# Kernel optimization log

Hardware: AMD Instinct MI355X
Metric: run time of the kernel (lower is better)

Reference implementation:

```python
import jax, jax.numpy as jnp
from jax import lax
import numpy as np

B, C, N, MAX_OUT = 8, 16, 2048, 100


def setup_inputs() -> dict:
    key = jax.random.key(0)
    kc, kw, ks = jax.random.split(key, 3)
    # well-formed xyxy boxes: centers in [0,1000), sizes in [1,101)
    ctr = jax.random.uniform(kc, (B, N, 2), jnp.float32) * 1000.0
    wh = jax.random.uniform(kw, (B, N, 2), jnp.float32) * 100.0 + 1.0
    boxes = jnp.concatenate([ctr - wh * 0.5, ctr + wh * 0.5], axis=-1)  # [B,N,4]
    scores = jax.random.uniform(ks, (B, C, N), jnp.float32)  # [B,C,N]
    return {
        "boxes": boxes,
        "scores": scores,
        "max_output_boxes_per_class": MAX_OUT,
        "iou_threshold": jnp.array([0.5], jnp.float32),
        "score_threshold": jnp.array([0.5], jnp.float32),
    }


def _pairwise_iou(bx):
    # bx: [N,4] xyxy -> [N,N] IoU (matches torchvision.ops.box_iou)
    x1, y1, x2, y2 = bx[:, 0], bx[:, 1], bx[:, 2], bx[:, 3]
    area = (x2 - x1) * (y2 - y1)
    iw = jnp.clip(jnp.minimum(x2[:, None], x2[None, :]) - jnp.maximum(x1[:, None], x1[None, :]), 0.0)
    ih = jnp.clip(jnp.minimum(y2[:, None], y2[None, :]) - jnp.maximum(y1[:, None], y1[None, :]), 0.0)
    inter = iw * ih
    return inter / (area[:, None] + area[None, :] - inter)


def _nms_selected(boxes, scores, iou_threshold, score_threshold, max_out):
    # boxes [B,N,4], scores [B,C,N]
    b, c, n = scores.shape
    iou = jax.vmap(_pairwise_iou)(boxes)  # [B,N,N], shared across classes
    iou_t = iou_threshold.reshape(())
    score_t = score_threshold.reshape(())

    def one_class(iou_b, cls_scores):
        order = jnp.argsort(-cls_scores)          # descending score order [N]
        valid = cls_scores[order] > score_t       # strict >, as in the torch code

        def step(suppressed, inp):
            ok, bi = inp
            kept = ok & (~suppressed[bi])
            # greedy suppression: a kept box removes all boxes with IoU > thr
            suppressed = suppressed | (kept & (iou_b[bi] > iou_t))
            return suppressed, kept

        _, keep = lax.scan(step, jnp.zeros((n,), bool), (valid, order))
        rank = jnp.cumsum(keep.astype(jnp.int32)) - 1
        sel = keep & (rank < max_out)
        pos = jnp.where(sel, rank, max_out)  # overflow/non-selected -> dropped slot
        buf = jnp.full((max_out + 1,), -1, jnp.int32).at[pos].set(
            jnp.where(sel, order.astype(jnp.int32), -1))
        return buf[:max_out]  # box indices in score order, -1 padded

    per_bc = jax.vmap(lambda iou_b, sb: jax.vmap(lambda s: one_class(iou_b, s))(sb))(iou, scores)  # [B,C,max_out]
    b_idx = jnp.broadcast_to(jnp.arange(b, dtype=jnp.int32)[:, None, None], per_bc.shape)
    c_idx = jnp.broadcast_to(jnp.arange(c, dtype=jnp.int32)[None, :, None], per_bc.shape)
    rows = jnp.stack([b_idx, c_idx, per_bc], axis=-1).reshape(-1, 3)  # [B*C*max_out, 3]
    # invalid (padded) rows are all -1
    return jnp.where(rows[:, 2:3] >= 0, rows, -1)


def reference(boxes, scores, max_output_boxes_per_class, iou_threshold, score_threshold):
    return _nms_selected(boxes, scores, iou_threshold, score_threshold,
                         int(max_output_boxes_per_class))
```

## Files before the change

kernel.cpp:

```cpp
#include <hip/hip_runtime.h>
#include <stdint.h>


#define NBOX 2048
#define THREADS 1024
#define CHUNK 128
#define MAXKEEP 256

__global__ __launch_bounds__(THREADS) void nms_kernel(
    const float* __restrict__ boxes,
    const float* __restrict__ scores,
    const int* __restrict__ maxOutPtr,
    const float* __restrict__ iouThrPtr,
    const float* __restrict__ scoreThrPtr,
    int* __restrict__ out,
    int B, int C, int slots)
{
  __shared__ unsigned long long skeys[NBOX];
  __shared__ float sx1[NBOX], sy1[NBOX], sx2[NBOX], sy2[NBOX], sar[NBOX];
  __shared__ unsigned colmask[CHUNK][4];
  __shared__ unsigned char suppPre[CHUNK];
  __shared__ int keptPos[MAXKEEP];
  __shared__ int Vsh, cntSh;

  const int tid  = threadIdx.x;
  const int lane = tid & 63;
  const int wave = tid >> 6;
  const int bc = blockIdx.x;
  const int b = bc / C, c = bc % C;
  const float iouT   = iouThrPtr[0];
  const float scoreT = scoreThrPtr[0];
  int mOut = maxOutPtr[0];
  if (mOut > slots) mOut = slots;
  if (mOut > MAXKEEP) mOut = MAXKEEP;
  if (mOut < 0) mOut = 0;

  const float* cls = scores + ((size_t)b * C + c) * NBOX;
  if (tid == 0) { Vsh = 0; cntSh = 0; }
  __syncthreads();

  {
    float s0 = cls[tid], s1 = cls[tid + 1024];
    unsigned u0 = __float_as_uint(s0); u0 = (u0 & 0x80000000u) ? ~u0 : (u0 | 0x80000000u);
    unsigned u1 = __float_as_uint(s1); u1 = (u1 & 0x80000000u) ? ~u1 : (u1 | 0x80000000u);
    skeys[tid]        = ((unsigned long long)u0 << 32) | (0xFFFFFFFFu - (unsigned)tid);
    skeys[tid + 1024] = ((unsigned long long)u1 << 32) | (0xFFFFFFFFu - (unsigned)(tid + 1024));
    unsigned long long m0 = __ballot(s0 > scoreT);
    unsigned long long m1 = __ballot(s1 > scoreT);
    if (lane == 0) atomicAdd(&Vsh, __popcll(m0) + __popcll(m1));
  }

  for (unsigned k = 2; k <= NBOX; k <<= 1) {
    for (unsigned s = k >> 1; s > 0; s >>= 1) {
      __syncthreads();
      unsigned i = ((tid & ~(s - 1)) << 1) | (tid & (s - 1));
      unsigned j = i | s;
      unsigned long long a = skeys[i], bb = skeys[j];
      bool up = ((i & k) == 0);
      bool sw = up ? (a < bb) : (a > bb);
      if (sw) { skeys[i] = bb; skeys[j] = a; }
    }
  }
  __syncthreads();
  const int V = Vsh;

  const float4* bx = (const float4*)boxes + (size_t)b * NBOX;
  for (int p = tid; p < V; p += THREADS) {
    int idx = (int)(0xFFFFFFFFu - (unsigned)skeys[p]);
    float4 f = bx[idx];
    sx1[p] = f.x; sy1[p] = f.y; sx2[p] = f.z; sy2[p] = f.w;
    sar[p] = (f.z - f.x) * (f.w - f.y);
  }
  __syncthreads();

  int cnt = 0;
  for (int s0 = 0; s0 < V && cnt < mOut; s0 += CHUNK) {
    int clen = V - s0; if (clen > CHUNK) clen = CHUNK;

    if (tid < CHUNK * 4) ((unsigned*)colmask)[tid] = 0;
    if (tid < CHUNK) suppPre[tid] = 0;
    __syncthreads();

    {
      int qo = tid & (CHUNK - 1);
      int ko = tid >> 7;
      if (qo < clen) {
        int q = s0 + qo;
        float qx1 = sx1[q], qy1 = sy1[q], qx2 = sx2[q], qy2 = sy2[q], qa = sar[q];
        int hit = 0;
        for (int k = ko; k < cnt; k += 8) {
          int kp = keptPos[k];
          float iw = fminf(sx2[kp], qx2) - fmaxf(sx1[kp], qx1);
          float ih = fminf(sy2[kp], qy2) - fmaxf(sy1[kp], qy1);
          iw = fmaxf(iw, 0.0f); ih = fmaxf(ih, 0.0f);
          float inter = iw * ih;
          float iou = inter / (sar[kp] + qa - inter);
          if (iou > iouT) hit = 1;
        }
        if (hit) suppPre[qo] = 1;
      }
    }

    {
      int i = tid & (CHUNK - 1);
      if (i < clen) {
        int ip = s0 + i;
        float ix1 = sx1[ip], iy1 = sy1[ip], ix2 = sx2[ip], iy2 = sy2[ip], ia = sar[ip];
        for (int j = tid >> 7; j < clen; j += 8) {
          if (j <= i) continue;
          int q = s0 + j;
          float iw = fminf(ix2, sx2[q]) - fmaxf(ix1, sx1[q]);
          float ih = fminf(iy2, sy2[q]) - fmaxf(iy1, sy1[q]);
          iw = fmaxf(iw, 0.0f); ih = fmaxf(ih, 0.0f);
          float inter = iw * ih;
          float iou = inter / (ia + sar[q] - inter);
          if (iou > iouT) atomicOr(&colmask[j][i >> 5], 1u << (i & 31));
        }
      }
    }
    __syncthreads();

    if (wave == 0) {
      unsigned a0 = colmask[lane][0], a1 = colmask[lane][1];
      unsigned a2 = colmask[lane][2], a3 = colmask[lane][3];
      unsigned b0 = colmask[lane + 64][0], b1 = colmask[lane + 64][1];
      unsigned b2 = colmask[lane + 64][2], b3 = colmask[lane + 64][3];
      int supA = suppPre[lane];
      int supB = suppPre[lane + 64];
      int cl = cnt;
      for (int r = 0; r < clen && cl < mOut; ++r) {
        int v = (r < 64) ? supA : supB;
        int isSup = __shfl(v, r & 63);
        if (!isSup) {
          if (lane == 0) keptPos[cl] = s0 + r;
          cl++;
          unsigned w = r >> 5, bit = r & 31;
          unsigned av = (w == 0) ? a0 : (w == 1) ? a1 : (w == 2) ? a2 : a3;
          unsigned bv = (w == 0) ? b0 : (w == 1) ? b1 : (w == 2) ? b2 : b3;
          supA |= (av >> bit) & 1;
          supB |= (bv >> bit) & 1;
        }
      }
      if (lane == 0) cntSh = cl;
    }
    __syncthreads();
    cnt = cntSh;
  }

  int base = bc * slots * 3;
  for (int s = tid; s < slots; s += THREADS) {
    int v = -1;
    if (s < cnt) {
      int p = keptPos[s];
      v = (int)(0xFFFFFFFFu - (unsigned)skeys[p]);
    }
    out[base + s * 3 + 0] = (v >= 0) ? b : -1;
    out[base + s * 3 + 1] = (v >= 0) ? c : -1;
    out[base + s * 3 + 2] = v;
  }
}

extern "C" void kernel_launch(void* const* d_in, const int* in_sizes, int n_in,
                              void* d_out, int out_size, void* d_ws, size_t ws_size,
                              hipStream_t stream) {
  const float* boxes  = (const float*)d_in[0];
  const float* scores = (const float*)d_in[1];
  const int*   maxOut = (const int*)d_in[2];
  const float* iouT   = (const float*)d_in[3];
  const float* scoreT = (const float*)d_in[4];
  int* out = (int*)d_out;

  const int N = NBOX;
  int B = in_sizes[0] / (4 * N);
  int C = in_sizes[1] / (B * N);
  int slots = out_size / (B * C * 3);

  nms_kernel<<<dim3(B * C), dim3(THREADS), 0, stream>>>(
      boxes, scores, maxOut, iouT, scoreT, out, B, C, slots);
}
```

Measured before the change: 93.71 us.

## Replace shared-memory bitonic sort stages with register shuffle stages

The bitonic sort of score keys now keeps each thread's two elements in registers and does every compare-exchange with stride 64 or less through cross-lane shuffles. Only strides of 128 and above go through shared memory with block barriers. This cuts the number of __syncthreads and LDS round trips in the sort from about 66 to a handful per merge level. The cost is more shuffle instructions on 64-bit values and a more intricate index mapping, where each wave owns a 128-element segment.

Result: no change. 92.85 us (-0.9%).

```diff
diff --git a/kernel.cpp b/kernel.cpp
--- a/kernel.cpp
+++ b/kernel.cpp
@@ -6,6 +6,16 @@
 #define THREADS 1024
 #define CHUNK 128
 #define MAXKEEP 256
+
+typedef unsigned long long u64;
+
+__device__ __forceinline__ u64 ce_x(u64 v, int s, bool up, int lane) {
+  u64 p = __shfl_xor(v, s, 64);
+  bool lower = ((lane & s) == 0);
+  u64 mx = v > p ? v : p;
+  u64 mn = v > p ? p : v;
+  return (up == lower) ? mx : mn;
+}
 
 __global__ __launch_bounds__(THREADS) void nms_kernel(
     const float* __restrict__ boxes,
@@ -16,7 +26,7 @@
     int* __restrict__ out,
     int B, int C, int slots)
 {
-  __shared__ unsigned long long skeys[NBOX];
+  __shared__ u64 skeys[NBOX];
   __shared__ float sx1[NBOX], sy1[NBOX], sx2[NBOX], sy2[NBOX], sar[NBOX];
   __shared__ unsigned colmask[CHUNK][4];
   __shared__ unsigned char suppPre[CHUNK];
@@ -25,7 +35,7 @@
 
   const int tid  = threadIdx.x;
   const int lane = tid & 63;
-  const int wave = tid >> 6;
+  const int w    = tid >> 6;
   const int bc = blockIdx.x;
   const int b = bc / C, c = bc % C;
   const float iouT   = iouThrPtr[0];
@@ -37,31 +47,63 @@
 
   const float* cls = scores + ((size_t)b * C + c) * NBOX;
   if (tid == 0) { Vsh = 0; cntSh = 0; }
+
+  const int j0 = w * 128 + lane;
+  const int j1 = j0 + 64;
+  float s0 = cls[j0], s1 = cls[j1];
+  unsigned u0 = __float_as_uint(s0); u0 = (u0 & 0x80000000u) ? ~u0 : (u0 | 0x80000000u);
+  unsigned u1 = __float_as_uint(s1); u1 = (u1 & 0x80000000u) ? ~u1 : (u1 | 0x80000000u);
+  u64 e0 = ((u64)u0 << 32) | (0xFFFFFFFFu - (unsigned)j0);
+  u64 e1 = ((u64)u1 << 32) | (0xFFFFFFFFu - (unsigned)j1);
+  int pop = __popcll(__ballot(s0 > scoreT)) + __popcll(__ballot(s1 > scoreT));
+
+  #pragma unroll
+  for (int k = 2; k <= 64; k <<= 1) {
+    #pragma unroll
+    for (int s = k >> 1; s >= 1; s >>= 1) {
+      bool up0 = ((lane & k) == 0);
+      bool up1 = (((64 + lane) & k) == 0);
+      e0 = ce_x(e0, s, up0, lane);
+      e1 = ce_x(e1, s, up1, lane);
+    }
+  }
+  {
+    bool up = ((w & 1) == 0);
+    u64 mx = e0 > e1 ? e0 : e1, mn = e0 > e1 ? e1 : e0;
+    e0 = up ? mx : mn; e1 = up ? mn : mx;
+    #pragma unroll
+    for (int s = 32; s >= 1; s >>= 1) {
+      e0 = ce_x(e0, s, up, lane);
+      e1 = ce_x(e1, s, up, lane);
+    }
+  }
+  skeys[j0] = e0; skeys[j1] = e1;
   __syncthreads();
-
-  {
-    float s0 = cls[tid], s1 = cls[tid + 1024];
-    unsigned u0 = __float_as_uint(s0); u0 = (u0 & 0x80000000u) ? ~u0 : (u0 | 0x80000000u);
-    unsigned u1 = __float_as_uint(s1); u1 = (u1 & 0x80000000u) ? ~u1 : (u1 | 0x80000000u);
-    skeys[tid]        = ((unsigned long long)u0 << 32) | (0xFFFFFFFFu - (unsigned)tid);
-    skeys[tid + 1024] = ((unsigned long long)u1 << 32) | (0xFFFFFFFFu - (unsigned)(tid + 1024));
-    unsigned long long m0 = __ballot(s0 > scoreT);
-    unsigned long long m1 = __ballot(s1 > scoreT);
-    if (lane == 0) atomicAdd(&Vsh, __popcll(m0) + __popcll(m1));
-  }
-
-  for (unsigned k = 2; k <= NBOX; k <<= 1) {
-    for (unsigned s = k >> 1; s > 0; s >>= 1) {
+  if (lane == 0) atomicAdd(&Vsh, pop);
+
+  for (int k = 256; k <= NBOX; k <<= 1) {
+    for (int s = k >> 1; s >= 128; s >>= 1) {
+      unsigned i = ((tid & ~(s - 1)) << 1) | (tid & (s - 1));
+      unsigned jj = i | (unsigned)s;
+      u64 a = skeys[i], bb = skeys[jj];
+      bool up = ((i & (unsigned)k) == 0);
+      bool sw = up ? (a < bb) : (a > bb);
+      if (sw) { skeys[i] = bb; skeys[jj] = a; }
       __syncthreads();
-      unsigned i = ((tid & ~(s - 1)) << 1) | (tid & (s - 1));
-      unsigned j = i | s;
-      unsigned long long a = skeys[i], bb = skeys[j];
-      bool up = ((i & k) == 0);
-      bool sw = up ? (a < bb) : (a > bb);
-      if (sw) { skeys[i] = bb; skeys[j] = a; }
-    }
-  }
-  __syncthreads();
+    }
+    e0 = skeys[j0]; e1 = skeys[j1];
+    bool up = (((unsigned)(w * 128) & (unsigned)k) == 0);
+    u64 mx = e0 > e1 ? e0 : e1, mn = e0 > e1 ? e1 : e0;
+    e0 = up ? mx : mn; e1 = up ? mn : mx;
+    #pragma unroll
+    for (int s = 32; s >= 1; s >>= 1) {
+      e0 = ce_x(e0, s, up, lane);
+      e1 = ce_x(e1, s, up, lane);
+    }
+    skeys[j0] = e0; skeys[j1] = e1;
+    __syncthreads();
+  }
+
   const int V = Vsh;
 
   const float4* bx = (const float4*)boxes + (size_t)b * NBOX;
@@ -74,8 +116,8 @@
   __syncthreads();
 
   int cnt = 0;
-  for (int s0 = 0; s0 < V && cnt < mOut; s0 += CHUNK) {
-    int clen = V - s0; if (clen > CHUNK) clen = CHUNK;
+  for (int c0 = 0; c0 < V && cnt < mOut; c0 += CHUNK) {
+    int clen = V - c0; if (clen > CHUNK) clen = CHUNK;
 
     if (tid < CHUNK * 4) ((unsigned*)colmask)[tid] = 0;
     if (tid < CHUNK) suppPre[tid] = 0;
@@ -85,7 +127,7 @@
       int qo = tid & (CHUNK - 1);
       int ko = tid >> 7;
       if (qo < clen) {
-        int q = s0 + qo;
+        int q = c0 + qo;
         float qx1 = sx1[q], qy1 = sy1[q], qx2 = sx2[q], qy2 = sy2[q], qa = sar[q];
         int hit = 0;
         for (int k = ko; k < cnt; k += 8) {
@@ -104,11 +146,11 @@
     {
       int i = tid & (CHUNK - 1);
       if (i < clen) {
-        int ip = s0 + i;
+        int ip = c0 + i;
         float ix1 = sx1[ip], iy1 = sy1[ip], ix2 = sx2[ip], iy2 = sy2[ip], ia = sar[ip];
         for (int j = tid >> 7; j < clen; j += 8) {
           if (j <= i) continue;
-          int q = s0 + j;
+          int q = c0 + j;
           float iw = fminf(ix2, sx2[q]) - fmaxf(ix1, sx1[q]);
           float ih = fminf(iy2, sy2[q]) - fmaxf(iy1, sy1[q]);
           iw = fmaxf(iw, 0.0f); ih = fmaxf(ih, 0.0f);
@@ -120,7 +162,7 @@
     }
     __syncthreads();
 
-    if (wave == 0) {
+    if (w == 0) {
       unsigned a0 = colmask[lane][0], a1 = colmask[lane][1];
       unsigned a2 = colmask[lane][2], a3 = colmask[lane][3];
       unsigned b0 = colmask[lane + 64][0], b1 = colmask[lane + 64][1];
@@ -132,11 +174,11 @@
         int v = (r < 64) ? supA : supB;
         int isSup = __shfl(v, r & 63);
         if (!isSup) {
-          if (lane == 0) keptPos[cl] = s0 + r;
+          if (lane == 0) keptPos[cl] = c0 + r;
           cl++;
-          unsigned w = r >> 5, bit = r & 31;
-          unsigned av = (w == 0) ? a0 : (w == 1) ? a1 : (w == 2) ? a2 : a3;
-          unsigned bv = (w == 0) ? b0 : (w == 1) ? b1 : (w == 2) ? b2 : b3;
+          unsigned wd = r >> 5, bit = r & 31;
+          unsigned av = (wd == 0) ? a0 : (wd == 1) ? a1 : (wd == 2) ? a2 : a3;
+          unsigned bv = (wd == 0) ? b0 : (wd == 1) ? b1 : (wd == 2) ? b2 : b3;
           supA |= (av >> bit) & 1;
           supB |= (bv >> bit) & 1;
         }
```
